# Optimization experiments

Hardware: AMD Instinct MI355X
Metric: run time of the kernel (lower is better)

The kernel has to match this reference:

```python
import jax, jax.numpy as jnp
import numpy as np

B, Hg, Wg, K, D, SD = 4, 128, 128, 16, 256, 64
N = Hg * Wg
MGAT_R0 = 1.5
TV_W = 1e-3
BIG_NEG = -10000.0
LN_EPS = 1e-5
# (r, s0, sl, cb) per geodesic scale
SCALES = ((1.5, 0.25, 0.2, 0.7), (2.5, 0.35, 0.2, 0.5), (4.0, 0.55, 0.25, 0.3))


def _build_grid_knn(H, W, Kn):
    # K nearest grid offsets (incl. self), deterministic tie-break
    cand = [(dy, dx) for dy in range(-3, 4) for dx in range(-3, 4)]
    cand.sort(key=lambda o: (o[0] * o[0] + o[1] * o[1], o[0], o[1]))
    offs = np.array(cand[:Kn])                                  # (K,2)
    ii, jj = np.meshgrid(np.arange(H), np.arange(W), indexing='ij')
    pos = np.stack([ii.ravel(), jj.ravel()], -1)                # (N,2)
    nb = pos[:, None, :] + offs[None]                           # (N,K,2)
    nb[..., 0] = np.clip(nb[..., 0], 0, H - 1)
    nb[..., 1] = np.clip(nb[..., 1], 0, W - 1)
    idx = (nb[..., 0] * W + nb[..., 1]).astype(np.int32)        # (N,K)
    rel = (nb - pos[:, None, :]).astype(np.float32)             # (N,K,2)
    geod = np.sqrt((rel ** 2).sum(-1)).astype(np.float32)       # (N,K)
    rel = rel / np.clip(np.abs(rel).max(axis=(0, 1), keepdims=True), 1e-6, None)
    return idx, rel, geod


def _lin(key, fan_in, fan_out):
    kw, kb = jax.random.split(key)
    s = 1.0 / np.sqrt(fan_in)
    return (jax.random.uniform(kw, (fan_in, fan_out), jnp.float32, -s, s),
            jax.random.uniform(kb, (fan_out,), jnp.float32, -s, s))


def setup_inputs() -> dict:
    key = jax.random.key(0)
    ks = jax.random.split(key, 14)
    idx, rel, geod = _build_grid_knn(Hg, Wg, K)
    inp = {
        'z': jax.random.normal(ks[0], (B, N, D), jnp.float32),
        'S': jax.random.normal(ks[1], (B, N, SD), jnp.float32),
        'rel': jnp.asarray(rel), 'geod': jnp.asarray(geod), 'idx': jnp.asarray(idx),
    }
    inp['Wq'], inp['bq'] = _lin(ks[2], D, D)
    inp['Wk'], inp['bk'] = _lin(ks[3], D, D)
    inp['Wv'], inp['bv'] = _lin(ks[4], D, D)
    inp['Wo'], inp['bo'] = _lin(ks[5], D, D)
    inp['ln_g'] = jnp.ones((D,), jnp.float32)
    inp['ln_b'] = jnp.zeros((D,), jnp.float32)
    inp['Ws1'], inp['bs1'] = _lin(ks[6], 2, 16)
    inp['Ws2'], inp['bs2'] = _lin(ks[7], 16, 16)
    inp['Wzg'], inp['bzg'] = _lin(ks[8], D, 16)
    inp['Wph'], inp['bph'] = _lin(ks[9], 32, 3)
    inp['Wsg'], inp['bsg'] = _lin(ks[10], 32, 3)
    return inp


def _forward(z, S, rel, geod, Wq, bq, Wk, bk, Wv, bv, Wo, bo, ln_g, ln_b,
             Ws1, bs1, Ws2, bs2, Wzg, bzg, Wph, bph, Wsg, bsg, idx):
    gelu = lambda x: jax.nn.gelu(x, approximate=False)
    q = z @ Wq + bq
    k = z @ Wk + bk
    v = z @ Wv + bv
    kN = k[:, idx]                                   # (B,N,K,D) neighbor gather
    vN = v[:, idx]                                   # (B,N,K,D)
    S_n = S[:, idx]                                  # (B,N,K,SD)
    m1 = S.mean(-1, keepdims=True)
    m2 = (S * S).mean(-1, keepdims=True)
    s_emb = gelu(gelu(jnp.concatenate([m1, m2], -1) @ Ws1 + bs1) @ Ws2 + bs2)
    z_emb = gelu(z @ Wzg + bzg)
    ker_in = jnp.concatenate([s_emb, z_emb], -1)     # (B,N,32)
    abc = ker_in @ Wph + bph                         # (B,N,3)
    La = jnp.exp(abc[..., 0]); Lb = abc[..., 1]; Lc = jnp.exp(abc[..., 2])
    # A = L L^T with L = [[La,0],[Lb,Lc]] -> symmetric 2x2 per node
    A00 = La * La; A01 = La * Lb; A11 = Lb * Lb + Lc * Lc   # (B,N)
    r0 = rel[None, ..., 0]; r1 = rel[None, ..., 1]          # (1,N,K)
    rAr = (A00[..., None] * r0 * r0 + 2.0 * A01[..., None] * r0 * r1
           + A11[..., None] * r1 * r1)                      # (B,N,K)
    sim = jnp.einsum('bns,bnks->bnk', S, S_n)
    content = jnp.einsum('bnd,bnkd->bnk', q, kN) / np.sqrt(D).astype(np.float32)
    g = jax.nn.softmax(ker_in @ Wsg + bsg, axis=-1)         # (B,N,3)
    geod_b = geod[None]                                     # (1,N,K)
    center_prior = jnp.exp(-geod_b ** 2 / MGAT_R0 ** 2)
    att_logits = jnp.zeros_like(content)
    for i, (r, s0, sl, cb) in enumerate(SCALES):
        hard_mask = (geod > r).astype(z.dtype)[None]
        sigma2 = jnp.maximum((s0 + sl * geod_b) ** 2, 1e-6)
        att_i = (content - rAr / sigma2 - 0.25 * geod_b + 1.0 * sim
                 + cb * center_prior + hard_mask * BIG_NEG)
        att_logits = att_logits + att_i * g[..., i:i + 1]
    att = jax.nn.softmax(att_logits, axis=-1)               # (B,N,K)
    agg = jnp.einsum('bnk,bnkd->bnd', att, vN)
    h = z + (agg @ Wo + bo)                                 # dropout/drop_path = identity (eval)
    mu = h.mean(-1, keepdims=True)
    var = ((h - mu) ** 2).mean(-1, keepdims=True)
    out = ln_g * (h - mu) / jnp.sqrt(var + LN_EPS) + ln_b
    # TV regularizer on Frobenius norm of A over the HxW grid
    A_norm = jnp.sqrt(A00 * A00 + 2.0 * A01 * A01 + A11 * A11).reshape(B, Hg, Wg)
    dy = jnp.abs(A_norm[:, 1:, :] - A_norm[:, :-1, :]).mean()
    dx = jnp.abs(A_norm[:, :, 1:] - A_norm[:, :, :-1]).mean()
    reg = TV_W * (dx + dy)
    return out, reg


def reference(z, S, rel, geod, idx, Wq, bq, Wk, bk, Wv, bv, Wo, bo, ln_g, ln_b,
              Ws1, bs1, Ws2, bs2, Wzg, bzg, Wph, bph, Wsg, bsg):
    return _forward(z, S, rel, geod, Wq, bq, Wk, bk, Wv, bv, Wo, bo, ln_g, ln_b,
                    Ws1, bs1, Ws2, bs2, Wzg, bzg, Wph, bph, Wsg, bsg, idx)
```

## Files before the change

### kernel.cpp

```cpp
#include <hip/hip_runtime.h>
#include <hip/hip_bf16.h>
#include <math.h>


typedef unsigned short u16;
typedef __attribute__((ext_vector_type(8))) short short8;
typedef __attribute__((ext_vector_type(4))) float f32x4;

#define NB 16384
#define NROWS 65536
#define DD 256
#define SDD 64

__device__ __forceinline__ float b2f(u16 u) {
  union { unsigned int i; float f; } c; c.i = ((unsigned int)u) << 16; return c.f;
}
__device__ __forceinline__ float blo(unsigned int u) {
  union { unsigned int i; float f; } c; c.i = u << 16; return c.f;
}
__device__ __forceinline__ float bhi(unsigned int u) {
  union { unsigned int i; float f; } c; c.i = u & 0xFFFF0000u; return c.f;
}
__device__ __forceinline__ u16 f2b(float f) {
  union { float f; unsigned int i; } c; c.f = f;
  unsigned int i = c.i;
  return (u16)((i + 0x7FFFu + ((i >> 16) & 1u)) >> 16);
}
__device__ __forceinline__ float gelu_exact(float x) {
  return 0.5f * x * (1.0f + erff(x * 0.70710678118654752f));
}
__device__ __forceinline__ void gll16(const u16* g, u16* l) {
  __builtin_amdgcn_global_load_lds(
      (const __attribute__((address_space(1))) void*)g,
      (__attribute__((address_space(3))) void*)l, 16, 0, 0);
}

__global__ __launch_bounds__(256) void k_prep_w(
    const float* __restrict__ Wq, const float* __restrict__ Wk,
    const float* __restrict__ Wv, const float* __restrict__ Wo,
    const float* __restrict__ Wzg,
    const float* __restrict__ bq, const float* __restrict__ bk,
    const float* __restrict__ bv, const float* __restrict__ bzg,
    u16* __restrict__ WqkvT, u16* __restrict__ WoT, float* __restrict__ biasq)
{
  int gid = blockIdx.x * 256 + threadIdx.x;
  int stride = gridDim.x * 256;
  for (int e = gid; e < 229376; e += stride) {
    int j = e >> 8, kk = e & 255;
    float v;
    if (j < 256)      v = Wq[kk * 256 + j];
    else if (j < 512) v = Wk[kk * 256 + (j - 256)];
    else if (j < 768) v = Wv[kk * 256 + (j - 512)];
    else if (j < 784) v = Wzg[kk * 16 + (j - 768)];
    else              v = 0.0f;
    WqkvT[e] = f2b(v);
  }
  for (int e = gid; e < 65536; e += stride) {
    int j = e >> 8, kk = e & 255;
    WoT[e] = f2b(Wo[kk * 256 + j]);
  }
  for (int e = gid; e < 784; e += stride)
    biasq[e] = e < 256 ? bq[e] : e < 512 ? bk[e - 256]
             : e < 768 ? bv[e - 512] : bzg[e - 768];
}

__global__ __launch_bounds__(256) void k_pre(
    const float* __restrict__ z, const float* __restrict__ S,
    u16* __restrict__ zb, float* __restrict__ rowdat)
{
  int w = threadIdx.x >> 6, t = threadIdx.x & 63;
  int r = blockIdx.x * 4 + w;
  float4 zv = *(const float4*)(z + (size_t)r * DD + t * 4);
  *(ushort4*)(zb + (size_t)r * DD + t * 4) =
      make_ushort4(f2b(zv.x), f2b(zv.y), f2b(zv.z), f2b(zv.w));
  float sv = S[(size_t)r * SDD + t];
  float s1 = sv, s2 = sv * sv;
  #pragma unroll
  for (int o = 32; o; o >>= 1) { s1 += __shfl_xor(s1, o); s2 += __shfl_xor(s2, o); }
  if (t == 0) {
    rowdat[(size_t)r * 8 + 0] = s1 * (1.0f / 64.0f);
    rowdat[(size_t)r * 8 + 1] = s2 * (1.0f / 64.0f);
  }
}

__global__ __launch_bounds__(256) void k_mfma_qkv(
    const u16* __restrict__ A, const u16* __restrict__ BT,
    const float* __restrict__ biasq,
    u16* __restrict__ qb, u16* __restrict__ kb, u16* __restrict__ vb,
    float* __restrict__ ze)
{
  __shared__ u16 As[128 * 64];
  __shared__ u16 Bs[128 * 64];
  int t = threadIdx.x, wv = t >> 6, lane = t & 63;
  int m0 = blockIdx.x * 128, j0 = blockIdx.y * 128;
  int wm = (wv & 1) * 64, wn = (wv >> 1) * 64;
  int quad = lane >> 4, l15 = lane & 15;
  int srow = lane >> 3, scol = (lane & 7) * 8;
  f32x4 acc[4][4] = {};
  for (int kc = 0; kc < 256; kc += 64) {
    if (kc) __syncthreads();
    for (int it = 0; it < 4; ++it) {
      int c = it * 4 + wv;
      gll16(A + (size_t)(m0 + c * 8 + srow) * 256 + kc + scol, As + c * 512);
      gll16(BT + (size_t)(j0 + c * 8 + srow) * 256 + kc + scol, Bs + c * 512);
    }
    __syncthreads();
    #pragma unroll
    for (int ks = 0; ks < 64; ks += 32) {
      short8 af[4], bfr[4];
      #pragma unroll
      for (int mi = 0; mi < 4; ++mi)
        af[mi] = *(const short8*)&As[(wm + mi * 16 + l15) * 64 + ks + quad * 8];
      #pragma unroll
      for (int ni = 0; ni < 4; ++ni)
        bfr[ni] = *(const short8*)&Bs[(wn + ni * 16 + l15) * 64 + ks + quad * 8];
      #pragma unroll
      for (int mi = 0; mi < 4; ++mi)
        #pragma unroll
        for (int ni = 0; ni < 4; ++ni)
          acc[mi][ni] = __builtin_amdgcn_mfma_f32_16x16x32_bf16(
              af[mi], bfr[ni], acc[mi][ni], 0, 0, 0);
    }
  }
  if (j0 < 768) {
    u16* obuf = (j0 < 256) ? qb : (j0 < 512) ? kb : vb;
    int jb = j0 & 255;
    #pragma unroll
    for (int ni = 0; ni < 4; ++ni) {
      int gcol = j0 + wn + ni * 16 + l15;
      float bia = biasq[gcol];
      int colb = jb + wn + ni * 16 + l15;
      #pragma unroll
      for (int mi = 0; mi < 4; ++mi) {
        int grow = m0 + wm + mi * 16 + quad * 4;
        #pragma unroll
        for (int r = 0; r < 4; ++r)
          obuf[(size_t)(grow + r) * 256 + colb] = f2b(acc[mi][ni][r] + bia);
      }
    }
  } else if (wn == 0) {
    float bia = biasq[768 + l15];
    #pragma unroll
    for (int mi = 0; mi < 4; ++mi) {
      int grow = m0 + wm + mi * 16 + quad * 4;
      #pragma unroll
      for (int r = 0; r < 4; ++r)
        ze[(size_t)(grow + r) * 16 + l15] = gelu_exact(acc[mi][0][r] + bia);
    }
  }
}

__global__ __launch_bounds__(256) void k_post(
    const float* __restrict__ ze,
    const float* __restrict__ Ws1, const float* __restrict__ bs1,
    const float* __restrict__ Ws2, const float* __restrict__ bs2,
    const float* __restrict__ Wph, const float* __restrict__ bph,
    const float* __restrict__ Wsg, const float* __restrict__ bsg,
    float* __restrict__ rowdat)
{
  __shared__ float h1s[16][17];
  __shared__ float kin[16][33];
  __shared__ float abcs[16][8];
  int rloc = threadIdx.x >> 4, j = threadIdx.x & 15;
  int r = blockIdx.x * 16 + rloc;
  float m1 = rowdat[(size_t)r * 8 + 0];
  float m2 = rowdat[(size_t)r * 8 + 1];
  h1s[rloc][j] = gelu_exact(m1 * Ws1[j] + m2 * Ws1[16 + j] + bs1[j]);
  __syncthreads();
  float h2 = bs2[j];
  #pragma unroll
  for (int i = 0; i < 16; ++i) h2 += h1s[rloc][i] * Ws2[i * 16 + j];
  kin[rloc][j] = gelu_exact(h2);
  kin[rloc][16 + j] = ze[(size_t)r * 16 + j];
  __syncthreads();
  if (j < 6) {
    int c = j % 3;
    const float* Wp = (j < 3) ? Wph : Wsg;
    const float* bp = (j < 3) ? bph : bsg;
    float a = bp[c];
    #pragma unroll
    for (int i = 0; i < 32; ++i) a += kin[rloc][i] * Wp[i * 3 + c];
    abcs[rloc][j] = a;
  }
  __syncthreads();
  if (j == 0) {
    float La = expf(abcs[rloc][0]), Lb = abcs[rloc][1], Lc = expf(abcs[rloc][2]);
    float A00 = La * La, A01 = La * Lb, A11 = Lb * Lb + Lc * Lc;
    float g0 = abcs[rloc][3], g1 = abcs[rloc][4], g2 = abcs[rloc][5];
    float gm = fmaxf(g0, fmaxf(g1, g2));
    float e0 = expf(g0 - gm), e1 = expf(g1 - gm), e2 = expf(g2 - gm);
    float inv = 1.0f / (e0 + e1 + e2);
    float* rd = rowdat + (size_t)r * 8;
    rd[0] = A00; rd[1] = A01; rd[2] = A11;
    rd[3] = e0 * inv; rd[4] = e1 * inv; rd[5] = e2 * inv;
    rd[6] = sqrtf(A00 * A00 + 2.0f * A01 * A01 + A11 * A11);
  }
}

__global__ __launch_bounds__(256) void k_attn(
    const u16* __restrict__ q, const u16* __restrict__ k,
    const u16* __restrict__ v, const float* __restrict__ S,
    const float* __restrict__ rel, const float* __restrict__ geod,
    const int* __restrict__ idx, const float* __restrict__ rowdat,
    u16* __restrict__ agg)
{
  __shared__ float qs[4][256];
  __shared__ float ss[4][64];
  int w = threadIdx.x >> 6, lane = threadIdx.x & 63;
  int r = blockIdx.x * 4 + w;
  int b = r >> 14, n = r & (NB - 1);

  {
    ushort4 q4 = *(const ushort4*)(q + (size_t)r * DD + lane * 4);
    qs[w][lane * 4 + 0] = b2f(q4.x) * 0.0625f;
    qs[w][lane * 4 + 1] = b2f(q4.y) * 0.0625f;
    qs[w][lane * 4 + 2] = b2f(q4.z) * 0.0625f;
    qs[w][lane * 4 + 3] = b2f(q4.w) * 0.0625f;
    ss[w][lane] = S[(size_t)r * SDD + lane];
  }
  __syncthreads();

  int g = lane >> 2, sub = lane & 3;
  int nbr = idx[n * 16 + g];
  size_t gidx = ((size_t)b << 14) + nbr;

  const u16* krow = k + gidx * DD;
  float p = 0.0f;
  #pragma unroll
  for (int c = 0; c < 8; ++c) {
    int e = (c * 4 + sub) * 8;
    uint2 ka = *(const uint2*)(krow + e);
    uint2 kb2 = *(const uint2*)(krow + e + 4);
    const float* qp = &qs[w][e];
    p += blo(ka.x) * qp[0] + bhi(ka.x) * qp[1]
       + blo(ka.y) * qp[2] + bhi(ka.y) * qp[3]
       + blo(kb2.x) * qp[4] + bhi(kb2.x) * qp[5]
       + blo(kb2.y) * qp[6] + bhi(kb2.y) * qp[7];
  }
  const float* Srow = S + gidx * SDD;
  #pragma unroll
  for (int c = 0; c < 4; ++c) {
    int e = sub * 16 + c * 4;
    float4 s4 = *(const float4*)(Srow + e);
    const float* sp = &ss[w][e];
    p += s4.x * sp[0] + s4.y * sp[1] + s4.z * sp[2] + s4.w * sp[3];
  }
  p += __shfl_xor(p, 1);
  p += __shfl_xor(p, 2);

  const float* rd = rowdat + (size_t)r * 8;
  float A00 = rd[0], A01 = rd[1], A11 = rd[2];
  float g0 = rd[3], g1 = rd[4], g2 = rd[5];
  float r0 = rel[(n * 16 + g) * 2];
  float r1 = rel[(n * 16 + g) * 2 + 1];
  float ge = geod[n * 16 + g];
  float rAr = A00 * r0 * r0 + 2.0f * A01 * r0 * r1 + A11 * r1 * r1;
  float prior = expf(-ge * ge * (1.0f / 2.25f));
  float lg = p - 0.25f * ge;
  { float s = 0.25f + 0.2f  * ge; float s2 = fmaxf(s * s, 1e-6f);
    lg += g0 * (-rAr / s2 + 0.7f * prior + (ge > 1.5f ? -10000.0f : 0.0f)); }
  { float s = 0.35f + 0.2f  * ge; float s2 = fmaxf(s * s, 1e-6f);
    lg += g1 * (-rAr / s2 + 0.5f * prior + (ge > 2.5f ? -10000.0f : 0.0f)); }
  { float s = 0.55f + 0.25f * ge; float s2 = fmaxf(s * s, 1e-6f);
    lg += g2 * (-rAr / s2 + 0.3f * prior + (ge > 4.0f ? -10000.0f : 0.0f)); }

  float m = lg;
  m = fmaxf(m, __shfl_xor(m, 4));
  m = fmaxf(m, __shfl_xor(m, 8));
  m = fmaxf(m, __shfl_xor(m, 16));
  m = fmaxf(m, __shfl_xor(m, 32));
  float e = expf(lg - m);
  float sm = e;
  sm += __shfl_xor(sm, 4);
  sm += __shfl_xor(sm, 8);
  sm += __shfl_xor(sm, 16);
  sm += __shfl_xor(sm, 32);
  float att = e / sm;

  float a0 = 0.f, a1 = 0.f, a2 = 0.f, a3 = 0.f;
  size_t bbase = (size_t)b << 14;
  #pragma unroll
  for (int kk = 0; kk < 16; ++kk) {
    float akk = __shfl(att, kk * 4);
    int nb2 = __shfl(nbr, kk * 4);
    const u16* vrow = v + (bbase + nb2) * DD;
    uint2 v4 = *(const uint2*)(vrow + lane * 4);
    a0 += akk * blo(v4.x);
    a1 += akk * bhi(v4.x);
    a2 += akk * blo(v4.y);
    a3 += akk * bhi(v4.y);
  }
  *(ushort4*)(agg + (size_t)r * DD + lane * 4) =
      make_ushort4(f2b(a0), f2b(a1), f2b(a2), f2b(a3));
}

__global__ __launch_bounds__(256) void k_mfma_out_ln(
    const u16* __restrict__ A, const u16* __restrict__ BT,
    const float* __restrict__ bo, const float* __restrict__ zres,
    const float* __restrict__ lng, const float* __restrict__ lnb,
    float* __restrict__ outp)
{
  __shared__ u16 As[128 * 64];
  __shared__ u16 Bs[256 * 64];
  int t = threadIdx.x, wv = t >> 6, lane = t & 63;
  int m0 = blockIdx.x * 128;
  int wm = wv * 32;
  int quad = lane >> 4, l15 = lane & 15;
  int srow = lane >> 3, scol = (lane & 7) * 8;
  f32x4 acc[2][16] = {};
  for (int kc = 0; kc < 256; kc += 64) {
    if (kc) __syncthreads();
    #pragma unroll
    for (int it = 0; it < 4; ++it) {
      int c = it * 4 + wv;
      gll16(A + (size_t)(m0 + c * 8 + srow) * 256 + kc + scol, As + c * 512);
    }
    #pragma unroll
    for (int it = 0; it < 8; ++it) {
      int c = it * 4 + wv;
      gll16(BT + (size_t)(c * 8 + srow) * 256 + kc + scol, Bs + c * 512);
    }
    __syncthreads();
    #pragma unroll
    for (int ks = 0; ks < 64; ks += 32) {
      short8 af[2], bfr[16];
      #pragma unroll
      for (int mi = 0; mi < 2; ++mi)
        af[mi] = *(const short8*)&As[(wm + mi * 16 + l15) * 64 + ks + quad * 8];
      #pragma unroll
      for (int ni = 0; ni < 16; ++ni)
        bfr[ni] = *(const short8*)&Bs[(ni * 16 + l15) * 64 + ks + quad * 8];
      #pragma unroll
      for (int mi = 0; mi < 2; ++mi)
        #pragma unroll
        for (int ni = 0; ni < 16; ++ni)
          acc[mi][ni] = __builtin_amdgcn_mfma_f32_16x16x32_bf16(
              af[mi], bfr[ni], acc[mi][ni], 0, 0, 0);
    }
  }
  float lg_[16], lb_[16], bo_[16];
  #pragma unroll
  for (int ni = 0; ni < 16; ++ni) {
    int col = ni * 16 + l15;
    lg_[ni] = lng[col]; lb_[ni] = lnb[col]; bo_[ni] = bo[col];
  }
  #pragma unroll
  for (int mi = 0; mi < 2; ++mi) {
    #pragma unroll
    for (int rr = 0; rr < 4; ++rr) {
      int row = m0 + wm + mi * 16 + quad * 4 + rr;
      float x[16];
      float s = 0.0f, sq = 0.0f;
      #pragma unroll
      for (int ni = 0; ni < 16; ++ni) {
        int col = ni * 16 + l15;
        float v = acc[mi][ni][rr] + bo_[ni] + zres[(size_t)row * 256 + col];
        x[ni] = v; s += v; sq += v * v;
      }
      #pragma unroll
      for (int o = 1; o < 16; o <<= 1) {
        s += __shfl_xor(s, o);
        sq += __shfl_xor(sq, o);
      }
      float mu = s * (1.0f / 256.0f);
      float var = sq * (1.0f / 256.0f) - mu * mu;
      float rstd = rsqrtf(var + 1e-5f);
      #pragma unroll
      for (int ni = 0; ni < 16; ++ni) {
        int col = ni * 16 + l15;
        outp[(size_t)row * 256 + col] = lg_[ni] * (x[ni] - mu) * rstd + lb_[ni];
      }
    }
  }
}

__global__ __launch_bounds__(256) void k_tv(
    const float* __restrict__ rowdat, float* __restrict__ sums)
{
  int gid = blockIdx.x * blockDim.x + threadIdx.x;
  int stride = gridDim.x * blockDim.x;
  float dy = 0.0f, dx = 0.0f;
  for (int e = gid; e < 4 * 127 * 128; e += stride) {
    int bb = e / 16256; int rem = e % 16256;
    int i = rem >> 7; int jj = rem & 127;
    int base = bb * 16384 + i * 128 + jj;
    dy += fabsf(rowdat[(size_t)(base + 128) * 8 + 6] - rowdat[(size_t)base * 8 + 6]);
  }
  for (int e = gid; e < 4 * 128 * 127; e += stride) {
    int bb = e / 16256; int rem = e % 16256;
    int i = rem / 127; int jj = rem % 127;
    int base = bb * 16384 + i * 128 + jj;
    dx += fabsf(rowdat[(size_t)(base + 1) * 8 + 6] - rowdat[(size_t)base * 8 + 6]);
  }
  #pragma unroll
  for (int o = 32; o; o >>= 1) { dy += __shfl_down(dy, o); dx += __shfl_down(dx, o); }
  if ((threadIdx.x & 63) == 0) {
    atomicAdd(&sums[0], dy);
    atomicAdd(&sums[1], dx);
  }
}

__global__ void k_reg(const float* __restrict__ sums, float* __restrict__ out)
{
  if (threadIdx.x == 0 && blockIdx.x == 0) {
    out[16777216] = 0.001f * (sums[0] + sums[1]) * (1.0f / 65024.0f);
  }
}

extern "C" void kernel_launch(void* const* d_in, const int* in_sizes, int n_in,
                              void* d_out, int out_size, void* d_ws, size_t ws_size,
                              hipStream_t stream)
{
  const float* z    = (const float*)d_in[0];
  const float* S    = (const float*)d_in[1];
  const float* rel  = (const float*)d_in[2];
  const float* geod = (const float*)d_in[3];
  const int*   idx  = (const int*)d_in[4];
  const float* Wq = (const float*)d_in[5];  const float* bq = (const float*)d_in[6];
  const float* Wk = (const float*)d_in[7];  const float* bk = (const float*)d_in[8];
  const float* Wv = (const float*)d_in[9];  const float* bv = (const float*)d_in[10];
  const float* Wo = (const float*)d_in[11]; const float* bo = (const float*)d_in[12];
  const float* lng = (const float*)d_in[13]; const float* lnb = (const float*)d_in[14];
  const float* Ws1 = (const float*)d_in[15]; const float* bs1 = (const float*)d_in[16];
  const float* Ws2 = (const float*)d_in[17]; const float* bs2 = (const float*)d_in[18];
  const float* Wzg = (const float*)d_in[19]; const float* bzg = (const float*)d_in[20];
  const float* Wph = (const float*)d_in[21]; const float* bph = (const float*)d_in[22];
  const float* Wsg = (const float*)d_in[23]; const float* bsg = (const float*)d_in[24];

  char* ws = (char*)d_ws;
  u16* zb = (u16*)ws;  ws += 33554432;
  u16* qb = (u16*)ws;  ws += 33554432;
  u16* kb = (u16*)ws;  ws += 33554432;
  u16* vb = (u16*)ws;  ws += 33554432;
  u16* WqkvT = (u16*)ws; ws += 458752;
  u16* WoT   = (u16*)ws; ws += 131072;
  float* biasq = (float*)ws; ws += 3136;
  float* ze    = (float*)ws; ws += 4194304;
  float* rowdat = (float*)ws; ws += 2097152;
  float* sums   = (float*)ws;
  u16* ab = zb;

  float* outp = (float*)d_out;

  hipMemsetAsync(sums, 0, 8, stream);
  k_prep_w<<<256, 256, 0, stream>>>(Wq, Wk, Wv, Wo, Wzg, bq, bk, bv, bzg,
                                    WqkvT, WoT, biasq);
  k_pre<<<NROWS / 4, 256, 0, stream>>>(z, S, zb, rowdat);
  k_mfma_qkv<<<dim3(512, 7), 256, 0, stream>>>(zb, WqkvT, biasq, qb, kb, vb, ze);
  k_post<<<NROWS / 16, 256, 0, stream>>>(ze, Ws1, bs1, Ws2, bs2,
                                         Wph, bph, Wsg, bsg, rowdat);
  k_attn<<<NROWS / 4, 256, 0, stream>>>(qb, kb, vb, S, rel, geod, idx, rowdat, ab);
  k_mfma_out_ln<<<512, 256, 0, stream>>>(ab, WoT, bo, z, lng, lnb, outp);
  k_tv<<<256, 256, 0, stream>>>(rowdat, sums);
  k_reg<<<1, 64, 0, stream>>>(sums, outp);
}
```

Before: 418.9 us.

## Tile attention over 4x4 grid patches with shared K/V halo and MFMA

Replaces the per-row gather attention with a tiled kernel. Each block handles a 4x4 patch of queries and loads an 8x8 halo of K, V and S into LDS. It computes dense 16x64 scores with bf16 MFMA, using a hi/lo bf16 split for the S similarity, scatters the masked softmax into a dense attention matrix, and aggregates V with MFMA. Neighbour offsets, relative positions and geodesic distances are derived from baked-in grid constants instead of reading idx/rel/geod. This depends on the fixed grid kNN structure and adds wasted MFMA work on non-neighbour columns.

```diff
diff --git a/kernel.cpp b/kernel.cpp
--- a/kernel.cpp
+++ b/kernel.cpp
@@ -4,6 +4,7 @@
 
 
 typedef unsigned short u16;
+typedef unsigned int u32;
 typedef __attribute__((ext_vector_type(8))) short short8;
 typedef __attribute__((ext_vector_type(4))) float f32x4;
 
@@ -33,6 +34,11 @@
   __builtin_amdgcn_global_load_lds(
       (const __attribute__((address_space(1))) void*)g,
       (__attribute__((address_space(3))) void*)l, 16, 0, 0);
+}
+__device__ __forceinline__ u32 qsc(u32 w) {
+  float lo = __uint_as_float(w << 16) * 0.0625f;
+  float hi = __uint_as_float(w & 0xFFFF0000u) * 0.0625f;
+  return (__float_as_uint(lo) >> 16) | (__float_as_uint(hi) & 0xFFFF0000u);
 }
 
 __global__ __launch_bounds__(256) void k_prep_w(
@@ -197,101 +203,213 @@
   }
 }
 
-__global__ __launch_bounds__(256) void k_attn(
+#define DYP 0x1004220331132212ULL
+#define DXP 0x0312402313123122ULL
+
+__global__ __launch_bounds__(256) void k_attn_mfma(
     const u16* __restrict__ q, const u16* __restrict__ k,
     const u16* __restrict__ v, const float* __restrict__ S,
-    const float* __restrict__ rel, const float* __restrict__ geod,
-    const int* __restrict__ idx, const float* __restrict__ rowdat,
-    u16* __restrict__ agg)
-{
-  __shared__ float qs[4][256];
-  __shared__ float ss[4][64];
-  int w = threadIdx.x >> 6, lane = threadIdx.x & 63;
-  int r = blockIdx.x * 4 + w;
-  int b = r >> 14, n = r & (NB - 1);
-
-  {
-    ushort4 q4 = *(const ushort4*)(q + (size_t)r * DD + lane * 4);
-    qs[w][lane * 4 + 0] = b2f(q4.x) * 0.0625f;
-    qs[w][lane * 4 + 1] = b2f(q4.y) * 0.0625f;
-    qs[w][lane * 4 + 2] = b2f(q4.z) * 0.0625f;
-    qs[w][lane * 4 + 3] = b2f(q4.w) * 0.0625f;
-    ss[w][lane] = S[(size_t)r * SDD + lane];
-  }
-  __syncthreads();
-
-  int g = lane >> 2, sub = lane & 3;
-  int nbr = idx[n * 16 + g];
-  size_t gidx = ((size_t)b << 14) + nbr;
-
-  const u16* krow = k + gidx * DD;
-  float p = 0.0f;
+    const float* __restrict__ rowdat, u16* __restrict__ aggp)
+{
+  __shared__ u16 KV[18432];
+  __shared__ u16 Qs[16 * 264];
+  __shared__ u16 Shi[64 * 72];
+  __shared__ u16 Slo[64 * 72];
+  __shared__ float scores[16 * 68];
+  __shared__ float attf[16 * 68];
+  __shared__ u16 attb[16 * 72];
+  __shared__ float rds[16 * 8];
+
+  int tid = threadIdx.x;
+  int bid = blockIdx.x;
+  int gidx = (bid & 7) * 512 + (bid >> 3);
+  int b = gidx >> 10;
+  int gid = gidx & 1023;
+  int gy0 = (gid >> 5) << 2, gx0 = (gid & 31) << 2;
+  int by0 = gy0 - 2; by0 = by0 < 0 ? 0 : (by0 > 120 ? 120 : by0);
+  int bx0 = gx0 - 2; bx0 = bx0 < 0 ? 0 : (bx0 > 120 ? 120 : bx0);
+  int oy = gy0 - by0, ox = gx0 - bx0;
+  size_t bbase = (size_t)b << 14;
+
+  int vpp = tid & 31, vdc = tid >> 5;
+  size_t vn0 = bbase + (size_t)(by0 + (vpp >> 2)) * 128 + bx0 + ((vpp & 3) * 2);
+  const u16* v0 = v + vn0 * 256;
+  uint4 va[4], vb4[4];
   #pragma unroll
-  for (int c = 0; c < 8; ++c) {
-    int e = (c * 4 + sub) * 8;
-    uint2 ka = *(const uint2*)(krow + e);
-    uint2 kb2 = *(const uint2*)(krow + e + 4);
-    const float* qp = &qs[w][e];
-    p += blo(ka.x) * qp[0] + bhi(ka.x) * qp[1]
-       + blo(ka.y) * qp[2] + bhi(ka.y) * qp[3]
-       + blo(kb2.x) * qp[4] + bhi(kb2.x) * qp[5]
-       + blo(kb2.y) * qp[6] + bhi(kb2.y) * qp[7];
-  }
-  const float* Srow = S + gidx * SDD;
-  #pragma unroll
-  for (int c = 0; c < 4; ++c) {
-    int e = sub * 16 + c * 4;
-    float4 s4 = *(const float4*)(Srow + e);
-    const float* sp = &ss[w][e];
-    p += s4.x * sp[0] + s4.y * sp[1] + s4.z * sp[2] + s4.w * sp[3];
-  }
-  p += __shfl_xor(p, 1);
-  p += __shfl_xor(p, 2);
-
-  const float* rd = rowdat + (size_t)r * 8;
-  float A00 = rd[0], A01 = rd[1], A11 = rd[2];
-  float g0 = rd[3], g1 = rd[4], g2 = rd[5];
-  float r0 = rel[(n * 16 + g) * 2];
-  float r1 = rel[(n * 16 + g) * 2 + 1];
-  float ge = geod[n * 16 + g];
-  float rAr = A00 * r0 * r0 + 2.0f * A01 * r0 * r1 + A11 * r1 * r1;
-  float prior = expf(-ge * ge * (1.0f / 2.25f));
-  float lg = p - 0.25f * ge;
-  { float s = 0.25f + 0.2f  * ge; float s2 = fmaxf(s * s, 1e-6f);
-    lg += g0 * (-rAr / s2 + 0.7f * prior + (ge > 1.5f ? -10000.0f : 0.0f)); }
-  { float s = 0.35f + 0.2f  * ge; float s2 = fmaxf(s * s, 1e-6f);
-    lg += g1 * (-rAr / s2 + 0.5f * prior + (ge > 2.5f ? -10000.0f : 0.0f)); }
-  { float s = 0.55f + 0.25f * ge; float s2 = fmaxf(s * s, 1e-6f);
-    lg += g2 * (-rAr / s2 + 0.3f * prior + (ge > 4.0f ? -10000.0f : 0.0f)); }
-
-  float m = lg;
-  m = fmaxf(m, __shfl_xor(m, 4));
-  m = fmaxf(m, __shfl_xor(m, 8));
-  m = fmaxf(m, __shfl_xor(m, 16));
-  m = fmaxf(m, __shfl_xor(m, 32));
-  float e = expf(lg - m);
-  float sm = e;
-  sm += __shfl_xor(sm, 4);
-  sm += __shfl_xor(sm, 8);
-  sm += __shfl_xor(sm, 16);
-  sm += __shfl_xor(sm, 32);
-  float att = e / sm;
-
-  float a0 = 0.f, a1 = 0.f, a2 = 0.f, a3 = 0.f;
-  size_t bbase = (size_t)b << 14;
-  #pragma unroll
-  for (int kk = 0; kk < 16; ++kk) {
-    float akk = __shfl(att, kk * 4);
-    int nb2 = __shfl(nbr, kk * 4);
-    const u16* vrow = v + (bbase + nb2) * DD;
-    uint2 v4 = *(const uint2*)(vrow + lane * 4);
-    a0 += akk * blo(v4.x);
-    a1 += akk * bhi(v4.x);
-    a2 += akk * blo(v4.y);
-    a3 += akk * bhi(v4.y);
-  }
-  *(ushort4*)(agg + (size_t)r * DD + lane * 4) =
-      make_ushort4(f2b(a0), f2b(a1), f2b(a2), f2b(a3));
+  for (int i = 0; i < 4; ++i) {
+    va[i]  = *(const uint4*)(v0 + (vdc + i * 8) * 8);
+    vb4[i] = *(const uint4*)(v0 + 256 + (vdc + i * 8) * 8);
+  }
+
+  {
+    int rr8 = tid >> 5, cc = tid & 31;
+    #pragma unroll
+    for (int p = 0; p < 8; ++p) {
+      size_t n = bbase + (size_t)(by0 + p) * 128 + bx0 + rr8;
+      uint4 ld = *(const uint4*)(k + n * 256 + cc * 8);
+      *(uint4*)&KV[(p * 8 + rr8) * 264 + cc * 8] = ld;
+    }
+    #pragma unroll
+    for (int p = 0; p < 2; ++p) {
+      int r = p * 8 + rr8;
+      size_t n = bbase + (size_t)(gy0 + (r >> 2)) * 128 + gx0 + (r & 3);
+      uint4 ld = *(const uint4*)(q + n * 256 + cc * 8);
+      uint4 o;
+      o.x = qsc(ld.x); o.y = qsc(ld.y); o.z = qsc(ld.z); o.w = qsc(ld.w);
+      *(uint4*)&Qs[r * 264 + cc * 8] = o;
+    }
+  }
+  {
+    int u = tid >> 2, qq = tid & 3;
+    size_t n = bbase + (size_t)(by0 + (u >> 3)) * 128 + bx0 + (u & 7);
+    const float* srow = S + n * 64 + qq * 16;
+    u32 hw[8], lw[8];
+    #pragma unroll
+    for (int i = 0; i < 4; ++i) {
+      float4 s4 = *(const float4*)(srow + i * 4);
+      u32 bx_ = __float_as_uint(s4.x), by_ = __float_as_uint(s4.y);
+      u32 bz_ = __float_as_uint(s4.z), bw_ = __float_as_uint(s4.w);
+      u32 hx = bx_ & 0xFFFF0000u, hy = by_ & 0xFFFF0000u;
+      u32 hz = bz_ & 0xFFFF0000u, hww = bw_ & 0xFFFF0000u;
+      hw[i * 2]     = (bx_ >> 16) | hy;
+      hw[i * 2 + 1] = (bz_ >> 16) | hww;
+      lw[i * 2]     = (__float_as_uint(s4.x - __uint_as_float(hx)) >> 16)
+                    | (__float_as_uint(s4.y - __uint_as_float(hy)) & 0xFFFF0000u);
+      lw[i * 2 + 1] = (__float_as_uint(s4.z - __uint_as_float(hz)) >> 16)
+                    | (__float_as_uint(s4.w - __uint_as_float(hww)) & 0xFFFF0000u);
+    }
+    *(uint4*)&Shi[u * 72 + qq * 16]     = make_uint4(hw[0], hw[1], hw[2], hw[3]);
+    *(uint4*)&Shi[u * 72 + qq * 16 + 8] = make_uint4(hw[4], hw[5], hw[6], hw[7]);
+    *(uint4*)&Slo[u * 72 + qq * 16]     = make_uint4(lw[0], lw[1], lw[2], lw[3]);
+    *(uint4*)&Slo[u * 72 + qq * 16 + 8] = make_uint4(lw[4], lw[5], lw[6], lw[7]);
+  }
+  if (tid < 128) {
+    int r = tid >> 3, sl = tid & 7;
+    size_t n = bbase + (size_t)(gy0 + (r >> 2)) * 128 + gx0 + (r & 3);
+    rds[tid] = rowdat[n * 8 + sl];
+  }
+  for (int i = tid; i < 16 * 68; i += 256) attf[i] = 0.0f;
+  __syncthreads();
+
+  int w = tid >> 6, lane = tid & 63, l15 = lane & 15, quad = lane >> 4;
+
+  {
+    f32x4 acc = {0.f, 0.f, 0.f, 0.f};
+    int arow = l15 * 264 + quad * 8;
+    int brow = (w * 16 + l15) * 264 + quad * 8;
+    #pragma unroll
+    for (int ks = 0; ks < 8; ++ks) {
+      short8 a  = *(const short8*)&Qs[arow + ks * 32];
+      short8 bq = *(const short8*)&KV[brow + ks * 32];
+      acc = __builtin_amdgcn_mfma_f32_16x16x32_bf16(a, bq, acc, 0, 0, 0);
+    }
+    int ucq = ((l15 >> 2) + oy) * 8 + (l15 & 3) + ox;
+    int sa = ucq * 72 + quad * 8;
+    int sb = (w * 16 + l15) * 72 + quad * 8;
+    #pragma unroll
+    for (int ks = 0; ks < 2; ++ks) {
+      short8 ah = *(const short8*)&Shi[sa + ks * 32];
+      short8 al = *(const short8*)&Slo[sa + ks * 32];
+      short8 bh = *(const short8*)&Shi[sb + ks * 32];
+      short8 bl = *(const short8*)&Slo[sb + ks * 32];
+      acc = __builtin_amdgcn_mfma_f32_16x16x32_bf16(ah, bh, acc, 0, 0, 0);
+      acc = __builtin_amdgcn_mfma_f32_16x16x32_bf16(ah, bl, acc, 0, 0, 0);
+      acc = __builtin_amdgcn_mfma_f32_16x16x32_bf16(al, bh, acc, 0, 0, 0);
+    }
+    #pragma unroll
+    for (int r4 = 0; r4 < 4; ++r4)
+      scores[(quad * 4 + r4) * 68 + w * 16 + l15] = acc[r4];
+  }
+  __syncthreads();
+
+  {
+    int r = tid >> 4, g = tid & 15;
+    int gy = gy0 + (r >> 2), gx = gx0 + (r & 3);
+    int dy = (int)((DYP >> (g * 4)) & 15) - 2;
+    int dx = (int)((DXP >> (g * 4)) & 15) - 2;
+    int ny = gy + dy; ny = ny < 0 ? 0 : (ny > 127 ? 127 : ny);
+    int nx = gx + dx; nx = nx < 0 ? 0 : (nx > 127 ? 127 : nx);
+    int cdy = ny - gy, cdx = nx - gx;
+    int u = (ny - by0) * 8 + (nx - bx0);
+    float sc = scores[r * 68 + u];
+    const float* rd = &rds[r * 8];
+    float A00 = rd[0], A01 = rd[1], A11 = rd[2];
+    float g0 = rd[3], g1 = rd[4], g2 = rd[5];
+    float r0 = cdy * 0.5f, r1 = cdx * 0.5f;
+    int ig2 = cdy * cdy + cdx * cdx;
+    float ge2 = (float)ig2;
+    float ge = sqrtf(ge2);
+    float rAr = A00 * r0 * r0 + 2.0f * A01 * r0 * r1 + A11 * r1 * r1;
+    float prior = __expf(-ge2 * (1.0f / 2.25f));
+    float lg = sc - 0.25f * ge;
+    { float s = 0.25f + 0.2f  * ge; float s2 = fmaxf(s * s, 1e-6f);
+      lg += g0 * (-rAr * __builtin_amdgcn_rcpf(s2) + 0.7f * prior
+                  + (ig2 >= 3  ? -10000.0f : 0.0f)); }
+    { float s = 0.35f + 0.2f  * ge; float s2 = fmaxf(s * s, 1e-6f);
+      lg += g1 * (-rAr * __builtin_amdgcn_rcpf(s2) + 0.5f * prior
+                  + (ig2 >= 7  ? -10000.0f : 0.0f)); }
+    { float s = 0.55f + 0.25f * ge; float s2 = fmaxf(s * s, 1e-6f);
+      lg += g2 * (-rAr * __builtin_amdgcn_rcpf(s2) + 0.3f * prior
+                  + (ig2 >= 17 ? -10000.0f : 0.0f)); }
+    float m = lg;
+    m = fmaxf(m, __shfl_xor(m, 1));
+    m = fmaxf(m, __shfl_xor(m, 2));
+    m = fmaxf(m, __shfl_xor(m, 4));
+    m = fmaxf(m, __shfl_xor(m, 8));
+    float e = __expf(lg - m);
+    float sm = e;
+    sm += __shfl_xor(sm, 1); sm += __shfl_xor(sm, 2);
+    sm += __shfl_xor(sm, 4); sm += __shfl_xor(sm, 8);
+    float att = e * __builtin_amdgcn_rcpf(sm);
+    atomicAdd(&attf[r * 68 + u], att);
+  }
+  __syncthreads();
+
+  {
+    int r = tid >> 4, c4 = (tid & 15) * 4;
+    float4 fv = *(const float4*)&attf[r * 68 + c4];
+    u32 w0 = (u32)f2b(fv.x) | ((u32)f2b(fv.y) << 16);
+    u32 w1 = (u32)f2b(fv.z) | ((u32)f2b(fv.w) << 16);
+    *(uint2*)&attb[r * 72 + c4] = make_uint2(w0, w1);
+  }
+  {
+    u32* VTw = (u32*)KV;
+    #pragma unroll
+    for (int i = 0; i < 4; ++i) {
+      int d0 = (vdc + i * 8) * 8;
+      u32 a0 = va[i].x, a1 = va[i].y, a2 = va[i].z, a3 = va[i].w;
+      u32 b0 = vb4[i].x, b1 = vb4[i].y, b2 = vb4[i].z, b3 = vb4[i].w;
+      VTw[(d0 + 0) * 36 + vpp] = (a0 & 0xFFFFu) | (b0 << 16);
+      VTw[(d0 + 1) * 36 + vpp] = (a0 >> 16)     | (b0 & 0xFFFF0000u);
+      VTw[(d0 + 2) * 36 + vpp] = (a1 & 0xFFFFu) | (b1 << 16);
+      VTw[(d0 + 3) * 36 + vpp] = (a1 >> 16)     | (b1 & 0xFFFF0000u);
+      VTw[(d0 + 4) * 36 + vpp] = (a2 & 0xFFFFu) | (b2 << 16);
+      VTw[(d0 + 5) * 36 + vpp] = (a2 >> 16)     | (b2 & 0xFFFF0000u);
+      VTw[(d0 + 6) * 36 + vpp] = (a3 & 0xFFFFu) | (b3 << 16);
+      VTw[(d0 + 7) * 36 + vpp] = (a3 >> 16)     | (b3 & 0xFFFF0000u);
+    }
+  }
+  __syncthreads();
+
+  {
+    short8 a0 = *(const short8*)&attb[l15 * 72 + quad * 8];
+    short8 a1 = *(const short8*)&attb[l15 * 72 + 32 + quad * 8];
+    #pragma unroll
+    for (int ni = 0; ni < 4; ++ni) {
+      int d = w * 64 + ni * 16 + l15;
+      f32x4 ag = {0.f, 0.f, 0.f, 0.f};
+      short8 bv0 = *(const short8*)&KV[d * 72 + quad * 8];
+      short8 bv1 = *(const short8*)&KV[d * 72 + 32 + quad * 8];
+      ag = __builtin_amdgcn_mfma_f32_16x16x32_bf16(a0, bv0, ag, 0, 0, 0);
+      ag = __builtin_amdgcn_mfma_f32_16x16x32_bf16(a1, bv1, ag, 0, 0, 0);
+      #pragma unroll
+      for (int r4 = 0; r4 < 4; ++r4) {
+        int row = quad * 4 + r4;
+        size_t n = bbase + (size_t)(gy0 + (row >> 2)) * 128 + gx0 + (row & 3);
+        aggp[n * 256 + d] = f2b(ag[r4]);
+      }
+    }
+  }
 }
 
 __global__ __launch_bounds__(256) void k_mfma_out_ln(
@@ -426,6 +544,7 @@
   const float* Wzg = (const float*)d_in[19]; const float* bzg = (const float*)d_in[20];
   const float* Wph = (const float*)d_in[21]; const float* bph = (const float*)d_in[22];
   const float* Wsg = (const float*)d_in[23]; const float* bsg = (const float*)d_in[24];
+  (void)rel; (void)geod; (void)idx;
 
   char* ws = (char*)d_ws;
   u16* zb = (u16*)ws;  ws += 33554432;
@@ -449,7 +568,7 @@
   k_mfma_qkv<<<dim3(512, 7), 256, 0, stream>>>(zb, WqkvT, biasq, qb, kb, vb, ze);
   k_post<<<NROWS / 16, 256, 0, stream>>>(ze, Ws1, bs1, Ws2, bs2,
                                          Wph, bph, Wsg, bsg, rowdat);
-  k_attn<<<NROWS / 4, 256, 0, stream>>>(qb, kb, vb, S, rel, geod, idx, rowdat, ab);
+  k_attn_mfma<<<4096, 256, 0, stream>>>(qb, kb, vb, S, rowdat, ab);
   k_mfma_out_ln<<<512, 256, 0, stream>>>(ab, WoT, bo, z, lng, lnb, outp);
   k_tv<<<256, 256, 0, stream>>>(rowdat, sums);
   k_reg<<<1, 64, 0, stream>>>(sums, outp);
```

New measurement: 376.3 us. -10.2%, faster.
